# Optimization experiments

Hardware: AMD Instinct MI355X
Metric: run time of the kernel (lower is better)

The kernel has to match this reference:

```python
import jax, jax.numpy as jnp
import numpy as np

N = 100000          # num nodes
E = 1600000         # num edges
D = 128             # input_dim == output_dim
H = 8               # heads
C = D // H          # per-head out channels (16)
NEG_SLOPE = 0.2     # PyG GATConv leaky_relu default
LN_EPS = 1e-5


def setup_inputs() -> dict:
    key = jax.random.key(0)
    ks = jax.random.split(key, 8)
    x = jax.random.normal(ks[0], (N, D), dtype=jnp.float32)
    edge_index = jax.random.randint(ks[1], (2, E), 0, N, dtype=jnp.int64)
    scale = 1.0 / np.sqrt(D)
    W = jax.random.normal(ks[2], (D, H * C), dtype=jnp.float32) * scale
    att_src = jax.random.normal(ks[3], (H, C), dtype=jnp.float32) * scale
    att_dst = jax.random.normal(ks[4], (H, C), dtype=jnp.float32) * scale
    bias = jnp.zeros((H * C,), dtype=jnp.float32)
    gamma = jnp.ones((D,), dtype=jnp.float32)
    beta = jnp.zeros((D,), dtype=jnp.float32)
    return {"x": x, "edge_index": edge_index, "W": W, "att_src": att_src,
            "att_dst": att_dst, "bias": bias, "gamma": gamma, "beta": beta}


def reference(x, edge_index, W, att_src, att_dst, bias, gamma, beta):
    src, dst = edge_index[0], edge_index[1]
    # linear transform -> [N, H, C]
    h = (x @ W).reshape(N, H, C)
    # per-node attention terms [N, H]
    a_src = jnp.einsum("nhc,hc->nh", h, att_src)
    a_dst = jnp.einsum("nhc,hc->nh", h, att_dst)
    # per-edge raw scores [E, H]
    e = a_src[src] + a_dst[dst]
    e = jnp.where(e >= 0, e, NEG_SLOPE * e)
    # segment softmax over destination neighborhoods
    m = jax.ops.segment_max(e, dst, num_segments=N)          # [N, H]
    e = jnp.exp(e - m[dst])
    s = jax.ops.segment_sum(e, dst, num_segments=N)          # [N, H]
    alpha = e / (s[dst] + 1e-16)                             # [E, H]
    # weighted scatter-aggregate of source features
    msg = h[src] * alpha[:, :, None]                         # [E, H, C]
    out = jax.ops.segment_sum(msg, dst, num_segments=N).reshape(N, H * C)
    out = out + bias
    # residual (input_dim == output_dim -> identity)
    out = out + x
    # LayerNorm
    mu = jnp.mean(out, axis=-1, keepdims=True)
    var = jnp.var(out, axis=-1, keepdims=True)
    out = (out - mu) * jax.lax.rsqrt(var + LN_EPS) * gamma + beta
    # ReLU (dropout is identity in eval)
    return jax.nn.relu(out)
```

## Files before the change

### kernel.cpp

```cpp
#include <hip/hip_runtime.h>
#include <hip/hip_fp16.h>

#define N_NODES 100000
#define N_EDGES 1600000
#define NEG_SLOPE 0.2f
#define LN_EPS 1e-5f
#define NB 782
#define GEMM_BLOCKS 782
#define BIN_BLOCKS 196
#define BIN_EDGES 8192
#define BUCKET_CAP 4096
#define CSR_CAP 2816

__global__ __launch_bounds__(256) void gemm_bin_kernel(const float* __restrict__ x,
                                                       const float* __restrict__ W,
                                                       const float* __restrict__ att_src,
                                                       const float* __restrict__ att_dst,
                                                       const int* __restrict__ ei,
                                                       __half* __restrict__ h16,
                                                       __half* __restrict__ a_srcp,
                                                       float* __restrict__ a_dstp,
                                                       int* __restrict__ bucket_cursor,
                                                       unsigned* __restrict__ binned) {
    __shared__ float xs[128 * 64];
    __shared__ float ws[64 * 128];
    const int t = threadIdx.x;

    if (blockIdx.x >= GEMM_BLOCKS) {
        int* hist = reinterpret_cast<int*>(xs);
        int* cbase = reinterpret_cast<int*>(ws);
        for (int i = t; i < NB; i += 256) hist[i] = 0;
        __syncthreads();
        const int e0 = (blockIdx.x - GEMM_BLOCKS) * BIN_EDGES;
        const int4* dsts = reinterpret_cast<const int4*>(ei + N_EDGES);
        const int b4 = e0 >> 2;
        for (int i = t; i < BIN_EDGES / 4; i += 256) {
            int idx = b4 + i;
            if (idx < N_EDGES / 4) {
                int4 d = dsts[idx];
                atomicAdd(&hist[d.x >> 7], 1);
                atomicAdd(&hist[d.y >> 7], 1);
                atomicAdd(&hist[d.z >> 7], 1);
                atomicAdd(&hist[d.w >> 7], 1);
            }
        }
        __syncthreads();
        for (int i = t; i < NB; i += 256) {
            int c = hist[i];
            cbase[i] = c ? atomicAdd(&bucket_cursor[i], c) : 0;
        }
        __syncthreads();
        for (int i = t; i < NB; i += 256) hist[i] = 0;
        __syncthreads();
        for (int i = t; i < BIN_EDGES; i += 256) {
            int e = e0 + i;
            if (e < N_EDGES) {
                int s_ = ei[e];
                int d = ei[N_EDGES + e];
                int bk = d >> 7;
                int off = atomicAdd(&hist[bk], 1);
                binned[bk * BUCKET_CAP + cbase[bk] + off] = (unsigned)((s_ << 7) | (d & 127));
            }
        }
        return;
    }

    const int nbase = blockIdx.x * 128;
    const int cx = (t & 15) * 8;
    const int ry = (t >> 4) * 8;
    float acc[8][8] = {};
    for (int kb = 0; kb < 2; ++kb) {
        __syncthreads();
        for (int i = t; i < 2048; i += 256) {
            int r = i >> 4, kq = i & 15;
            int gr = nbase + r;
            gr = gr < N_NODES ? gr : N_NODES - 1;
            *reinterpret_cast<float4*>(&xs[r * 64 + kq * 4]) =
                *reinterpret_cast<const float4*>(&x[(size_t)gr * 128 + kb * 64 + kq * 4]);
        }
        for (int i = t; i < 2048; i += 256) {
            int k = i >> 5, cq = i & 31;
            *reinterpret_cast<float4*>(&ws[k * 128 + cq * 4]) =
                *reinterpret_cast<const float4*>(&W[(size_t)(kb * 64 + k) * 128 + cq * 4]);
        }
        __syncthreads();
        for (int kq = 0; kq < 16; ++kq) {
            float4 xv[8];
            float4 wv[4][2];
#pragma unroll
            for (int r = 0; r < 8; ++r)
                xv[r] = *reinterpret_cast<const float4*>(&xs[(ry + r) * 64 + kq * 4]);
#pragma unroll
            for (int k2 = 0; k2 < 4; ++k2) {
                wv[k2][0] = *reinterpret_cast<const float4*>(&ws[(kq * 4 + k2) * 128 + cx]);
                wv[k2][1] = *reinterpret_cast<const float4*>(&ws[(kq * 4 + k2) * 128 + cx + 4]);
            }
#pragma unroll
            for (int r = 0; r < 8; ++r) {
                const float* xf = reinterpret_cast<const float*>(&xv[r]);
#pragma unroll
                for (int k2 = 0; k2 < 4; ++k2) {
                    const float xx = xf[k2];
                    const float* w0 = reinterpret_cast<const float*>(&wv[k2][0]);
                    const float* w1 = reinterpret_cast<const float*>(&wv[k2][1]);
#pragma unroll
                    for (int c = 0; c < 4; ++c) {
                        acc[r][c] = fmaf(xx, w0[c], acc[r][c]);
                        acc[r][c + 4] = fmaf(xx, w1[c], acc[r][c + 4]);
                    }
                }
            }
        }
    }
#pragma unroll
    for (int r = 0; r < 8; ++r) {
        int gr = nbase + ry + r;
        if (gr < N_NODES) {
            __half hb[8];
#pragma unroll
            for (int c = 0; c < 8; ++c) hb[c] = __float2half_rn(acc[r][c]);
            *reinterpret_cast<uint4*>(&h16[(size_t)gr * 128 + cx]) =
                *reinterpret_cast<const uint4*>(hb);
        }
    }

    float asv[8], adv[8];
#pragma unroll
    for (int c = 0; c < 8; ++c) {
        asv[c] = att_src[cx + c];
        adv[c] = att_dst[cx + c];
    }
    __syncthreads();
#pragma unroll
    for (int r = 0; r < 8; ++r) {
        float ps = 0.f, pd = 0.f;
#pragma unroll
        for (int c = 0; c < 8; ++c) {
            ps = fmaf(acc[r][c], asv[c], ps);
            pd = fmaf(acc[r][c], adv[c], pd);
        }
        xs[(ry + r) * 16 + (t & 15)] = ps;
        xs[2048 + (ry + r) * 16 + (t & 15)] = pd;
    }
    __syncthreads();
    for (int idx = t; idx < 1024; idx += 256) {
        int row = idx >> 3, hd = idx & 7;
        int gr = nbase + row;
        if (gr < N_NODES) {
            a_srcp[gr * 8 + hd] =
                __float2half_rn(xs[row * 16 + hd * 2] + xs[row * 16 + hd * 2 + 1]);
            a_dstp[gr * 8 + hd] = xs[2048 + row * 16 + hd * 2] + xs[2048 + row * 16 + hd * 2 + 1];
        }
    }
}

__global__ __launch_bounds__(256) void csr_build_kernel(const unsigned* __restrict__ binned,
                                                        const int* __restrict__ bucket_cursor,
                                                        int* __restrict__ row_beg,
                                                        int* __restrict__ row_end,
                                                        int* __restrict__ csr_src) {
    __shared__ int deg[128];
    __shared__ int sc[128];
    __shared__ int cur[128];
    __shared__ unsigned stage[CSR_CAP];
    const int b = blockIdx.x;
    const int t = threadIdx.x;
    const int pbase = b * BUCKET_CAP;
    const int cnt = bucket_cursor[b];
    const int n0 = b << 7;
    const bool fits = cnt <= CSR_CAP;
    if (t < 128) deg[t] = 0;
    __syncthreads();
    if (fits) {
        for (int i = t; i < cnt; i += 256) {
            unsigned p = binned[pbase + i];
            stage[i] = p;
            atomicAdd(&deg[p & 127], 1);
        }
    } else {
        for (int i = t; i < cnt; i += 256)
            atomicAdd(&deg[binned[pbase + i] & 127], 1);
    }
    __syncthreads();
    if (t < 128) sc[t] = deg[t];
    __syncthreads();
    for (int off = 1; off < 128; off <<= 1) {
        int u = (t < 128 && t >= off) ? sc[t - off] : 0;
        __syncthreads();
        if (t < 128) sc[t] += u;
        __syncthreads();
    }
    if (t < 128) {
        int excl = sc[t] - deg[t];
        cur[t] = excl;
        int n = n0 + t;
        if (n < N_NODES) {
            row_beg[n] = pbase + excl;
            row_end[n] = pbase + excl + deg[t];
        }
    }
    __syncthreads();
    if (fits) {
        for (int i = t; i < cnt; i += 256) {
            unsigned p = stage[i];
            int off = atomicAdd(&cur[p & 127], 1);
            csr_src[pbase + off] = (int)(p >> 7);
        }
    } else {
        for (int i = t; i < cnt; i += 256) {
            unsigned p = binned[pbase + i];
            int off = atomicAdd(&cur[p & 127], 1);
            csr_src[pbase + off] = (int)(p >> 7);
        }
    }
}

__global__ __launch_bounds__(256) void node_aggregate_kernel(const int* __restrict__ row_beg,
                                                             const int* __restrict__ row_end,
                                                             const int* __restrict__ csr_src,
                                                             const __half* __restrict__ h16,
                                                             const __half* __restrict__ a_srcp,
                                                             const float* __restrict__ a_dstp,
                                                             const float* __restrict__ x,
                                                             const float* __restrict__ bias,
                                                             const float* __restrict__ gamma,
                                                             const float* __restrict__ beta,
                                                             float* __restrict__ out) {
    int node = blockIdx.x * 4 + (threadIdx.x >> 6);
    if (node >= N_NODES) return;
    const int lane = threadIdx.x & 63;
    const int q = lane >> 4;
    const int ql = lane & 15;
    const int ch = ql * 8;
    const int head = ql >> 1;

    const float adst = a_dstp[node * 8 + head];

    const int beg = row_beg[node];
    const int end = row_end[node];

    float s = 0.f;
    float accv[8] = {};

    const char* __restrict__ hbase = reinterpret_cast<const char*>(h16);
    const unsigned chb = (unsigned)(ql * 16);

#define LOADH(dst_, sidx_) \
    dst_ = *reinterpret_cast<const uint4*>(hbase + ((unsigned)(sidx_) * 256u + chb))
#define LOADA(dst_, sidx_) dst_ = __half2float(a_srcp[(sidx_) * 8 + head])

#define CONSUME(hv_, av_)                                                  \
    {                                                                      \
        float e = (av_) + adst;                                            \
        e = fmaxf(e, NEG_SLOPE * e);                                       \
        e = fminf(e, 80.f);                                                \
        const float p = __expf(e);                                         \
        s += p;                                                            \
        const __half* hh = reinterpret_cast<const __half*>(&(hv_));        \
        _Pragma("unroll")                                                  \
        for (int j = 0; j < 8; ++j)                                        \
            accv[j] = fmaf(p, __half2float(hh[j]), accv[j]);               \
    }

#define REFILL(hv_, av_, iv_)                                              \
    {                                                                      \
        const int ic = inext < end ? inext : endm1;                        \
        const int sn = csr_src[ic];                                        \
        LOADH(hv_, sn);                                                    \
        LOADA(av_, sn);                                                    \
        iv_ = inext;                                                       \
        inext += 4;                                                        \
    }

    const int i0 = beg + q;
    if (i0 < end) {
        const int endm1 = end - 1;
        int iA = i0, iB = i0 + 4, iC = i0 + 8, iD = i0 + 12;
        const int cB = iB < end ? iB : endm1;
        const int cC = iC < end ? iC : endm1;
        const int cD = iD < end ? iD : endm1;
        const int sA = csr_src[iA];
        const int sB = csr_src[cB];
        const int sC = csr_src[cC];
        const int sD = csr_src[cD];
        uint4 hA, hB, hC, hD;
        float aA, aB, aC, aD;
        LOADH(hA, sA); LOADA(aA, sA);
        LOADH(hB, sB); LOADA(aB, sB);
        LOADH(hC, sC); LOADA(aC, sC);
        LOADH(hD, sD); LOADA(aD, sD);
        int inext = i0 + 16;
        for (;;) {
            CONSUME(hA, aA);
            REFILL(hA, aA, iA);
            if (iB >= end) break;
            CONSUME(hB, aB);
            REFILL(hB, aB, iB);
            if (iC >= end) break;
            CONSUME(hC, aC);
            REFILL(hC, aC, iC);
            if (iD >= end) break;
            CONSUME(hD, aD);
            REFILL(hD, aD, iD);
            if (iA >= end) break;
        }
    }
#undef LOADH
#undef LOADA
#undef CONSUME
#undef REFILL

    s += __shfl_xor(s, 16);
    s += __shfl_xor(s, 32);
#pragma unroll
    for (int j = 0; j < 8; ++j) {
        accv[j] += __shfl_xor(accv[j], 16);
        accv[j] += __shfl_xor(accv[j], 32);
    }

    const float rs = 1.0f / (s + 1e-16f);
    const float* xrp = x + (size_t)node * 128 + ch;
    float v[8];
#pragma unroll
    for (int j = 0; j < 8; ++j) {
        const float xr = __builtin_nontemporal_load(xrp + j);
        v[j] = accv[j] * rs + bias[ch + j] + xr;
    }

    float sum = 0.f, sq = 0.f;
#pragma unroll
    for (int j = 0; j < 8; ++j) {
        sum += v[j];
        sq = fmaf(v[j], v[j], sq);
    }
#pragma unroll
    for (int off = 32; off > 0; off >>= 1) {
        sum += __shfl_xor(sum, off);
        sq += __shfl_xor(sq, off);
    }
    const float mu = sum * (1.0f / 512.0f);
    const float var = sq * (1.0f / 512.0f) - mu * mu;
    const float inv = rsqrtf(var + LN_EPS);
    if (q == 0) {
        float o[8];
#pragma unroll
        for (int j = 0; j < 8; ++j) {
            float tt = (v[j] - mu) * inv * gamma[ch + j] + beta[ch + j];
            o[j] = tt > 0.f ? tt : 0.f;
        }
        float* op = out + (size_t)node * 128 + ch;
#pragma unroll
        for (int j = 0; j < 8; ++j) __builtin_nontemporal_store(o[j], op + j);
    }
}

extern "C" void kernel_launch(void* const* d_in, const int* in_sizes, int n_in,
                              void* d_out, int out_size, void* d_ws, size_t ws_size,
                              hipStream_t stream) {
    const float* x = (const float*)d_in[0];
    const int* ei = (const int*)d_in[1];
    const float* W = (const float*)d_in[2];
    const float* att_src = (const float*)d_in[3];
    const float* att_dst = (const float*)d_in[4];
    const float* bias = (const float*)d_in[5];
    const float* gamma = (const float*)d_in[6];
    const float* beta = (const float*)d_in[7];
    float* out = (float*)d_out;

    char* base = (char*)d_ws;
    __half* h16    = (__half*)base;
    __half* a_srcp = (__half*)(base + 25600000);
    float* a_dstp  = (float*)(base + 27200000);
    int* csr_src   = (int*)(base + 30400000);
    int* row_beg   = (int*)(base + 43212288);
    int* row_end   = (int*)(base + 43612288);
    unsigned* binned = (unsigned*)(base + 44012288);
    int* bucket_cursor = (int*)(base + 56824576);

    hipMemsetAsync(bucket_cursor, 0, NB * sizeof(int), stream);
    gemm_bin_kernel<<<GEMM_BLOCKS + BIN_BLOCKS, 256, 0, stream>>>(
        x, W, att_src, att_dst, ei, h16, a_srcp, a_dstp, bucket_cursor, binned);
    csr_build_kernel<<<NB, 256, 0, stream>>>(binned, bucket_cursor, row_beg, row_end, csr_src);
    node_aggregate_kernel<<<(N_NODES + 3) / 4, 256, 0, stream>>>(
        row_beg, row_end, csr_src, h16, a_srcp, a_dstp, x, bias, gamma, beta, out);
}
```

Baseline: 163.5 us.

## Compute node linear transform with fp16 MFMA instead of fp32 FMA tiles

Replaces the fp32 register-tiled GEMM in the fused gemm/bin kernel with fp16 MFMA 16x16x32 instructions. x is converted to fp16 in padded LDS and W is pre-swizzled into fragment layout. Results are staged back through LDS for coalesced h16 stores and for computing the attention dot products from fp16 h. The goal is to cut the ALU cost of the GEMM phase. In exchange, inputs are rounded to fp16 and a_src/a_dst are now computed from rounded h, which slightly lowers accuracy, and each block re-converts W.

```diff
diff --git a/kernel.cpp b/kernel.cpp
--- a/kernel.cpp
+++ b/kernel.cpp
@@ -12,6 +12,11 @@
 #define BUCKET_CAP 4096
 #define CSR_CAP 2816
 
+typedef _Float16 f16x8 __attribute__((ext_vector_type(8)));
+typedef float f32x4 __attribute__((ext_vector_type(4)));
+
+#define XLDS_LD 136
+
 __global__ __launch_bounds__(256) void gemm_bin_kernel(const float* __restrict__ x,
                                                        const float* __restrict__ W,
                                                        const float* __restrict__ att_src,
@@ -22,13 +27,12 @@
                                                        float* __restrict__ a_dstp,
                                                        int* __restrict__ bucket_cursor,
                                                        unsigned* __restrict__ binned) {
-    __shared__ float xs[128 * 64];
-    __shared__ float ws[64 * 128];
+    __shared__ __align__(16) char lds[34816 + 32768];
     const int t = threadIdx.x;
 
     if (blockIdx.x >= GEMM_BLOCKS) {
-        int* hist = reinterpret_cast<int*>(xs);
-        int* cbase = reinterpret_cast<int*>(ws);
+        int* hist = reinterpret_cast<int*>(lds);
+        int* cbase = reinterpret_cast<int*>(lds + 4096);
         for (int i = t; i < NB; i += 256) hist[i] = 0;
         __syncthreads();
         const int e0 = (blockIdx.x - GEMM_BLOCKS) * BIN_EDGES;
@@ -65,91 +69,85 @@
         return;
     }
 
+    _Float16* x_lds = reinterpret_cast<_Float16*>(lds);
+    _Float16* w_frag = reinterpret_cast<_Float16*>(lds + 34816);
     const int nbase = blockIdx.x * 128;
-    const int cx = (t & 15) * 8;
-    const int ry = (t >> 4) * 8;
-    float acc[8][8] = {};
-    for (int kb = 0; kb < 2; ++kb) {
-        __syncthreads();
-        for (int i = t; i < 2048; i += 256) {
-            int r = i >> 4, kq = i & 15;
-            int gr = nbase + r;
-            gr = gr < N_NODES ? gr : N_NODES - 1;
-            *reinterpret_cast<float4*>(&xs[r * 64 + kq * 4]) =
-                *reinterpret_cast<const float4*>(&x[(size_t)gr * 128 + kb * 64 + kq * 4]);
-        }
-        for (int i = t; i < 2048; i += 256) {
-            int k = i >> 5, cq = i & 31;
-            *reinterpret_cast<float4*>(&ws[k * 128 + cq * 4]) =
-                *reinterpret_cast<const float4*>(&W[(size_t)(kb * 64 + k) * 128 + cq * 4]);
-        }
-        __syncthreads();
-        for (int kq = 0; kq < 16; ++kq) {
-            float4 xv[8];
-            float4 wv[4][2];
-#pragma unroll
-            for (int r = 0; r < 8; ++r)
-                xv[r] = *reinterpret_cast<const float4*>(&xs[(ry + r) * 64 + kq * 4]);
-#pragma unroll
-            for (int k2 = 0; k2 < 4; ++k2) {
-                wv[k2][0] = *reinterpret_cast<const float4*>(&ws[(kq * 4 + k2) * 128 + cx]);
-                wv[k2][1] = *reinterpret_cast<const float4*>(&ws[(kq * 4 + k2) * 128 + cx + 4]);
-            }
-#pragma unroll
-            for (int r = 0; r < 8; ++r) {
-                const float* xf = reinterpret_cast<const float*>(&xv[r]);
-#pragma unroll
-                for (int k2 = 0; k2 < 4; ++k2) {
-                    const float xx = xf[k2];
-                    const float* w0 = reinterpret_cast<const float*>(&wv[k2][0]);
-                    const float* w1 = reinterpret_cast<const float*>(&wv[k2][1]);
-#pragma unroll
-                    for (int c = 0; c < 4; ++c) {
-                        acc[r][c] = fmaf(xx, w0[c], acc[r][c]);
-                        acc[r][c + 4] = fmaf(xx, w1[c], acc[r][c + 4]);
-                    }
-                }
-            }
-        }
-    }
-#pragma unroll
-    for (int r = 0; r < 8; ++r) {
-        int gr = nbase + ry + r;
-        if (gr < N_NODES) {
-            __half hb[8];
-#pragma unroll
-            for (int c = 0; c < 8; ++c) hb[c] = __float2half_rn(acc[r][c]);
-            *reinterpret_cast<uint4*>(&h16[(size_t)gr * 128 + cx]) =
-                *reinterpret_cast<const uint4*>(hb);
-        }
-    }
-
-    float asv[8], adv[8];
-#pragma unroll
-    for (int c = 0; c < 8; ++c) {
-        asv[c] = att_src[cx + c];
-        adv[c] = att_dst[cx + c];
-    }
-    __syncthreads();
-#pragma unroll
-    for (int r = 0; r < 8; ++r) {
-        float ps = 0.f, pd = 0.f;
-#pragma unroll
-        for (int c = 0; c < 8; ++c) {
-            ps = fmaf(acc[r][c], asv[c], ps);
-            pd = fmaf(acc[r][c], adv[c], pd);
-        }
-        xs[(ry + r) * 16 + (t & 15)] = ps;
-        xs[2048 + (ry + r) * 16 + (t & 15)] = pd;
-    }
-    __syncthreads();
+    const int w = t >> 6;
+    const int l = t & 63;
+    const int lr = l & 15;
+    const int lg = l >> 4;
+
+    for (int i = t; i < 2048; i += 256) {
+        int r = i >> 4, seg = i & 15;
+        int gr = nbase + r;
+        gr = gr < N_NODES ? gr : N_NODES - 1;
+        const float4 v0 = *reinterpret_cast<const float4*>(&x[(size_t)gr * 128 + seg * 8]);
+        const float4 v1 = *reinterpret_cast<const float4*>(&x[(size_t)gr * 128 + seg * 8 + 4]);
+        _Float16 hb[8] = {(_Float16)v0.x, (_Float16)v0.y, (_Float16)v0.z, (_Float16)v0.w,
+                          (_Float16)v1.x, (_Float16)v1.y, (_Float16)v1.z, (_Float16)v1.w};
+        *reinterpret_cast<uint4*>(&x_lds[r * XLDS_LD + seg * 8]) =
+            *reinterpret_cast<const uint4*>(hb);
+    }
+    for (int s = t; s < 2048; s += 256) {
+        int ks = s >> 9, ct = (s >> 6) & 7, ln = s & 63;
+        int kb = ks * 32 + (ln >> 4) * 8;
+        int col = ct * 16 + (ln & 15);
+        _Float16 wb[8];
+#pragma unroll
+        for (int j = 0; j < 8; ++j) wb[j] = (_Float16)W[(size_t)(kb + j) * 128 + col];
+        *reinterpret_cast<uint4*>(&w_frag[s * 8]) = *reinterpret_cast<const uint4*>(wb);
+    }
+    __syncthreads();
+
+    f32x4 acc[2][8] = {};
+    const int m0 = w * 32;
+#pragma unroll
+    for (int ks = 0; ks < 4; ++ks) {
+        f16x8 a[2], b[8];
+#pragma unroll
+        for (int rt = 0; rt < 2; ++rt)
+            a[rt] = *reinterpret_cast<const f16x8*>(
+                &x_lds[(m0 + rt * 16 + lr) * XLDS_LD + ks * 32 + lg * 8]);
+#pragma unroll
+        for (int ct = 0; ct < 8; ++ct)
+            b[ct] = *reinterpret_cast<const f16x8*>(&w_frag[((ks * 8 + ct) * 64 + l) * 8]);
+#pragma unroll
+        for (int rt = 0; rt < 2; ++rt)
+#pragma unroll
+            for (int ct = 0; ct < 8; ++ct)
+                acc[rt][ct] = __builtin_amdgcn_mfma_f32_16x16x32_f16(a[rt], b[ct],
+                                                                     acc[rt][ct], 0, 0, 0);
+    }
+    __syncthreads();
+#pragma unroll
+    for (int rt = 0; rt < 2; ++rt)
+#pragma unroll
+        for (int ct = 0; ct < 8; ++ct)
+#pragma unroll
+            for (int reg = 0; reg < 4; ++reg)
+                x_lds[(m0 + rt * 16 + lg * 4 + reg) * XLDS_LD + ct * 16 + lr] =
+                    (_Float16)acc[rt][ct][reg];
+    __syncthreads();
+    for (int i = t; i < 2048; i += 256) {
+        int r = i >> 4, seg = i & 15;
+        int gr = nbase + r;
+        if (gr < N_NODES)
+            *reinterpret_cast<uint4*>(&h16[(size_t)gr * 128 + seg * 8]) =
+                *reinterpret_cast<const uint4*>(&x_lds[r * XLDS_LD + seg * 8]);
+    }
     for (int idx = t; idx < 1024; idx += 256) {
         int row = idx >> 3, hd = idx & 7;
         int gr = nbase + row;
         if (gr < N_NODES) {
-            a_srcp[gr * 8 + hd] =
-                __float2half_rn(xs[row * 16 + hd * 2] + xs[row * 16 + hd * 2 + 1]);
-            a_dstp[gr * 8 + hd] = xs[2048 + row * 16 + hd * 2] + xs[2048 + row * 16 + hd * 2 + 1];
+            float ps = 0.f, pd = 0.f;
+#pragma unroll
+            for (int j = 0; j < 16; ++j) {
+                const float hv = (float)x_lds[row * XLDS_LD + hd * 16 + j];
+                ps = fmaf(hv, att_src[hd * 16 + j], ps);
+                pd = fmaf(hv, att_dst[hd * 16 + j], pd);
+            }
+            a_srcp[gr * 8 + hd] = __float2half_rn(ps);
+            a_dstp[gr * 8 + hd] = pd;
         }
     }
 }
```

New measurement: 147.4 us. 9.8% less time.
